# Optimization experiments

Measured on AMD Instinct MI355X. Metric: run time of the kernel, lower is better.

Reference implementation:

```python
import jax, jax.numpy as jnp
import numpy as np

B, C, H, W = 4, 288, 64, 64
P = 2
HEADS = 36
MLP_RATIO = 4.0
D = C * P * P              # hidden_size = 1152
HF = int(D * MLP_RATIO)    # 4608
LN_EPS = 1e-6
ATTN_EPS = 1e-8


def _layernorm(x):
    # LayerNorm over [C,H,W] per sample, no affine
    mu = jnp.mean(x, axis=(1, 2, 3), keepdims=True)
    var = jnp.mean((x - mu) ** 2, axis=(1, 2, 3), keepdims=True)
    return (x - mu) * jax.lax.rsqrt(var + LN_EPS)


def _seg(x):
    # b c (n1 p) (n2 p) -> b (n1 n2) (c p p)
    b, c, h, w = x.shape
    n1, n2 = h // P, w // P
    x = x.reshape(b, c, n1, P, n2, P).transpose(0, 2, 4, 1, 3, 5)
    return x.reshape(b, n1 * n2, c * P * P)


def _comb(t, h, w):
    # b (n1 n2) (c p p) -> b c (n1 p) (n2 p)
    b, n, dd = t.shape
    n1, n2 = h // P, w // P
    c = dd // (P * P)
    x = t.reshape(b, n1, n2, c, P, P).transpose(0, 3, 1, 4, 2, 5)
    return x.reshape(b, c, h, w)


def _lite_la(t, qkv_w, proj_w, proj_b):
    # ReLU-kernel linear attention with ones-padding normalization trick
    b, s, dm = t.shape
    d = dm // HEADS
    qkv = t @ qkv_w.T                       # [b,s,3*dm]
    q, k, v = jnp.split(qkv, 3, axis=-1)
    q = jax.nn.relu(q).reshape(b, s, HEADS, d)
    k = jax.nn.relu(k).reshape(b, s, HEADS, d)
    v = v.reshape(b, s, HEADS, d)
    v = jnp.concatenate([v, jnp.ones((b, s, HEADS, 1), v.dtype)], axis=-1)  # PAD_VAL=1
    vk = jnp.einsum('bshe,bshd->bhed', v, k)       # [b,h,d+1,d]
    out = jnp.einsum('bhed,bshd->bshe', vk, q)     # [b,s,h,d+1]
    out = out[..., :-1] / (out[..., -1:] + ATTN_EPS)
    return out.reshape(b, s, dm) @ proj_w.T + proj_b


def _glumb(t, inv_w, inv_b, dw_w, dw_b, pw_w):
    # GLU MBConv: 1x1 expand + SiLU -> 3x3 depthwise -> GLU gate -> 1x1 project
    b, n, c = t.shape
    hp = wp = int(n ** 0.5)
    x = t.reshape(b, hp, wp, c).transpose(0, 3, 1, 2)  # NCHW
    x = jnp.einsum('bchw,oc->bohw', x, inv_w[:, :, 0, 0]) + inv_b[None, :, None, None]
    x = jax.nn.silu(x)
    x = jax.lax.conv_general_dilated(x, dw_w, (1, 1), 'SAME',
                                     feature_group_count=dw_w.shape[0],
                                     dimension_numbers=('NCHW', 'OIHW', 'NCHW'))
    x = x + dw_b[None, :, None, None]
    x, gate = jnp.split(x, 2, axis=1)
    x = x * jax.nn.silu(gate)
    x = jnp.einsum('bchw,oc->bohw', x, pw_w[:, :, 0, 0])
    return x.reshape(b, c, n).transpose(0, 2, 1)


def setup_inputs() -> dict:
    key = jax.random.key(0)
    ks = jax.random.split(key, 10)
    s = 0.02
    return {
        'x': jax.random.normal(ks[0], (B, C, H, W), jnp.float32),
        'cond': jax.random.normal(ks[1], (B, 6 * C, H, W), jnp.float32),
        'global_token': jax.random.normal(ks[2], (B, D), jnp.float32),
        'time_token': jax.random.normal(ks[3], (B, D), jnp.float32),
        'ss_w': jax.random.normal(ks[4], (6 * C, 6 * C, 1, 1), jnp.float32) * s,
        'ss_b': jnp.zeros((6 * C,), jnp.float32),
        'qkv_w': jax.random.normal(ks[5], (3 * D, D), jnp.float32) * s,
        'proj_w': jax.random.normal(ks[6], (D, D), jnp.float32) * s,
        'proj_b': jnp.zeros((D,), jnp.float32),
        'inv_w': jax.random.normal(ks[7], (2 * HF, D, 1, 1), jnp.float32) * s,
        'inv_b': jnp.zeros((2 * HF,), jnp.float32),
        'dw_w': jax.random.normal(ks[8], (2 * HF, 1, 3, 3), jnp.float32) * s,
        'dw_b': jnp.zeros((2 * HF,), jnp.float32),
        'pw_w': jax.random.normal(ks[9], (D, HF, 1, 1), jnp.float32) * s,
    }


def reference(x, cond, global_token, time_token, ss_w, ss_b, qkv_w, proj_w, proj_b,
              inv_w, inv_b, dw_w, dw_b, pw_w):
    # scale_shift_table: SiLU + 1x1 conv on cond, chunk into 6 per-channel maps
    ss = jnp.einsum('bchw,oc->bohw', jax.nn.silu(cond), ss_w[:, :, 0, 0]) + ss_b[None, :, None, None]
    sh_msa, sc_msa, g_msa, sh_mlp, sc_mlp, g_mlp = jnp.split(ss, 6, axis=1)
    # attention branch
    tok = _seg(_layernorm(x) * (1.0 + sc_msa) + sh_msa)
    tok = jnp.concatenate([global_token[:, None], time_token[:, None], tok], axis=1)
    a = _lite_la(tok, qkv_w, proj_w, proj_b)
    x = x + _comb(a[:, 2:], H, W) * g_msa
    # MLP branch
    m = _glumb(_seg(_layernorm(x) * (1.0 + sc_mlp) + sh_mlp), inv_w, inv_b, dw_w, dw_b, pw_w)
    x = x + _comb(m, H, W) * g_mlp
    return x
```

## Files before the change

### kernel.cpp

```cpp
#include <hip/hip_runtime.h>
#include <hip/hip_bf16.h>
#include <cstdint>


typedef __bf16 bf16;
typedef bf16 bf16x8 __attribute__((ext_vector_type(8)));
typedef bf16 bf16x4 __attribute__((ext_vector_type(4)));
typedef float f32x4 __attribute__((ext_vector_type(4)));

typedef const __attribute__((address_space(1))) void gas_void;
typedef __attribute__((address_space(3))) void las_void;

__device__ __forceinline__ void gload16(const bf16* g, bf16* l) {
    __builtin_amdgcn_global_load_lds((gas_void*)g, (las_void*)l, 16, 0, 0);
}

#define BB 4
#define CC 288
#define HW 4096
#define C6 1728
#define DD 1152
#define SEQ 1026
#define RTOT 4104
#define NTOK 1024
#define HF 4608
#define HF2 9216
#define NPB 1179648

static constexpr size_t OFF_SUMS = 0;
static constexpr size_t OFF_SS   = 256;
static constexpr size_t SS_BYTES = (size_t)C6 * 16384 * 2;
static constexpr size_t OFF_R2   = OFF_SS + SS_BYTES;
static constexpr size_t OFF_PART1= OFF_R2;
static constexpr size_t OFF_A1   = OFF_R2;
static constexpr size_t OFF_T    = OFF_R2;
static constexpr size_t OFF_QKV  = OFF_T   + (size_t)RTOT*DD*2;
static constexpr size_t OFF_PART2= OFF_QKV;
static constexpr size_t OFF_VK   = OFF_QKV + (size_t)3456*RTOT*2;
static constexpr size_t OFF_ATT  = OFF_VK  + (size_t)144*1056*4;
static constexpr size_t OFF_APROJ= OFF_ATT + (size_t)RTOT*DD*2;
static constexpr size_t OFF_T2   = OFF_R2;
static constexpr size_t OFF_Y    = OFF_T2  + (size_t)4096*DD*2;
static constexpr size_t OFF_G    = OFF_Y   + (size_t)4096*HF2*2;
static constexpr size_t OFF_M    = OFF_G   + (size_t)4096*HF*2;
static constexpr size_t OFF_W    = OFF_R2  + 132120576;
static constexpr size_t OFF_WSS  = OFF_W;
static constexpr size_t OFF_WQKV = OFF_WSS  + (size_t)C6*C6*2;
static constexpr size_t OFF_WPROJ= OFF_WQKV + (size_t)3456*DD*2;
static constexpr size_t OFF_WINV = OFF_WPROJ+ (size_t)DD*DD*2;
static constexpr size_t OFF_WPW  = OFF_WINV + (size_t)HF2*DD*2;

__global__ __launch_bounds__(256) void cvt_bf16(const float* __restrict__ s,
                                                bf16* __restrict__ d, int n4) {
    int i = blockIdx.x * 256 + threadIdx.x;
    if (i < n4) {
        float4 v = ((const float4*)s)[i];
        bf16x4 o = {(bf16)v.x, (bf16)v.y, (bf16)v.z, (bf16)v.w};
        ((bf16x4*)d)[i] = o;
    }
}

__device__ __forceinline__ void block_reduce2_store(float s1, float s2, float* dst) {
    #pragma unroll
    for (int o = 32; o > 0; o >>= 1) { s1 += __shfl_down(s1, o); s2 += __shfl_down(s2, o); }
    __shared__ float r1[4], r2[4];
    int wave = threadIdx.x >> 6, lane = threadIdx.x & 63;
    if (lane == 0) { r1[wave] = s1; r2[wave] = s2; }
    __syncthreads();
    if (threadIdx.x == 0) {
        dst[0] = r1[0] + r1[1] + r1[2] + r1[3];
        dst[1] = r2[0] + r2[1] + r2[2] + r2[3];
    }
}

__global__ __launch_bounds__(256) void ln_stats(const float* __restrict__ x, float* __restrict__ part) {
    const float* base = x + (size_t)blockIdx.x * 4096;
    float s1 = 0.f, s2 = 0.f;
    #pragma unroll
    for (int it = 0; it < 4; it++) {
        float4 v = ((const float4*)base)[it * 256 + threadIdx.x];
        s1 += v.x + v.y + v.z + v.w;
        s2 += v.x * v.x + v.y * v.y + v.z * v.z + v.w * v.w;
    }
    block_reduce2_store(s1, s2, part + (size_t)blockIdx.x * 2);
}

__global__ __launch_bounds__(256) void reduce_part(const float* __restrict__ part, float* __restrict__ sums,
                                                   int nper, int out_off) {
    int b = blockIdx.x;
    float s1 = 0.f, s2 = 0.f;
    for (int i = threadIdx.x; i < nper; i += 256) {
        s1 += part[(size_t)(b * nper + i) * 2];
        s2 += part[(size_t)(b * nper + i) * 2 + 1];
    }
    block_reduce2_store(s1, s2, sums + out_off + b * 2);
}

__global__ __launch_bounds__(256) void prep_cond(const float* __restrict__ cond, bf16* __restrict__ A1) {
    __shared__ float tile[64][65];
    int b = blockIdx.z, k0 = blockIdx.y * 64, h0 = blockIdx.x * 64;
    int col = threadIdx.x & 63, r4 = threadIdx.x >> 6;
    const float* src = cond + ((size_t)b * C6 + k0) * HW + h0;
    #pragma unroll
    for (int p = 0; p < 16; p++) {
        int kk = r4 + p * 4;
        float v = src[(size_t)kk * HW + col];
        tile[col][kk] = v / (1.f + __expf(-v));
    }
    __syncthreads();
    bf16* dst = A1 + ((size_t)(b * HW + h0)) * C6 + k0;
    #pragma unroll
    for (int p = 0; p < 16; p++) {
        int rr = r4 + p * 4;
        dst[(size_t)rr * C6 + col] = (bf16)tile[rr][col];
    }
}

template <int EP, int BIAS>
__global__ __launch_bounds__(512, 2) void gemm256(const bf16* __restrict__ A, const bf16* __restrict__ B,
                                                  const float* __restrict__ bias, bf16* __restrict__ C,
                                                  int M, int N, int K, int reluLimit) {
    __shared__ __align__(16) bf16 As[2][256 * 64];
    __shared__ __align__(16) bf16 Bs[2][256 * 64];
    const int tid = threadIdx.x, wave = tid >> 6, lane = tid & 63;

    const int nx = gridDim.x, ny = gridDim.y, G = 8;
    int idx = blockIdx.y * nx + blockIdx.x;
    int total = nx * ny;
    int q = total >> 3, rm = total & 7;
    int xcd = idx & 7, slot = idx >> 3;
    int vid = (xcd < rm ? xcd * (q + 1) : rm * (q + 1) + (xcd - rm) * q) + slot;
    int band = vid / (G * nx);
    int r = vid - band * (G * nx);
    int gm = min(G, ny - band * G);
    const int m0 = (band * G + r % gm) * 256;
    const int n0 = (r / gm) * 256;

    const int srow_l = (wave << 3) + (lane >> 3);
    const int sk_el  = (((lane & 7) ^ (lane >> 3)) << 3);
    const bf16* pA[4]; const bf16* pB[4];
    #pragma unroll
    for (int g = 0; g < 4; ++g) {
        pA[g] = A + (size_t)min(m0 + g * 64 + srow_l, M - 1) * K + sk_el;
        pB[g] = B + (size_t)min(n0 + g * 64 + srow_l, N - 1) * K + sk_el;
    }
    auto STAGE_A = [&](int buf, int half) {
        #pragma unroll
        for (int rr = 0; rr < 2; ++rr) {
            gload16(pA[half * 2 + rr], &As[buf][half * 8192 + rr * 4096 + (wave << 9)]);
            pA[half * 2 + rr] += 64;
        }
    };
    auto STAGE_B = [&](int buf, int half) {
        #pragma unroll
        for (int rr = 0; rr < 2; ++rr) {
            gload16(pB[half * 2 + rr], &Bs[buf][half * 8192 + rr * 4096 + (wave << 9)]);
            pB[half * 2 + rr] += 64;
        }
    };

    const int wm_w = (wave >> 2) * 128, wn_w = (wave & 3) * 64;
    const int l15 = lane & 15;
    const int fswz = (l15 & 7) << 4;
    const int rk16 = (lane >> 4) << 4;

    bf16x8 af[8], bv[8];
    f32x4 acc[8][4];
    #pragma unroll
    for (int i = 0; i < 8; i++)
        #pragma unroll
        for (int j = 0; j < 4; j++) acc[i][j] = (f32x4){0.f, 0.f, 0.f, 0.f};

    auto LDA = [&](const bf16* base, int qm) {
        #pragma unroll
        for (int il = 0; il < 4; ++il)
            #pragma unroll
            for (int ks = 0; ks < 2; ++ks) {
                int row = wm_w + (qm * 4 + il) * 16 + l15;
                int kb  = (ks * 64 + rk16) ^ fswz;
                af[il * 2 + ks] = *(const bf16x8*)(base + row * 64 + (kb >> 1));
            }
    };
    auto LDB = [&](const bf16* base) {
        #pragma unroll
        for (int j = 0; j < 4; ++j)
            #pragma unroll
            for (int ks = 0; ks < 2; ++ks) {
                int row = wn_w + j * 16 + l15;
                int kb  = (ks * 64 + rk16) ^ fswz;
                bv[j * 2 + ks] = *(const bf16x8*)(base + row * 64 + (kb >> 1));
            }
    };
    auto MF = [&](int qm, int jh) {
        __builtin_amdgcn_s_setprio(1);
        #pragma unroll
        for (int il = 0; il < 4; ++il)
            #pragma unroll
            for (int jl = 0; jl < 2; ++jl)
                #pragma unroll
                for (int ks = 0; ks < 2; ++ks)
                    acc[qm * 4 + il][jh * 2 + jl] = __builtin_amdgcn_mfma_f32_16x16x32_bf16(
                        af[il * 2 + ks], bv[(jh * 2 + jl) * 2 + ks], acc[qm * 4 + il][jh * 2 + jl], 0, 0, 0);
        __builtin_amdgcn_s_setprio(0);
    };

    auto TILE = [&](int t, bool stage_next, bool last_vm) {
        const int cur = t & 1;
        const bf16* Ab = &As[cur][0];
        const bf16* Bb = &Bs[cur][0];
        LDA(Ab, 0);
        LDB(Bb);
        asm volatile("s_waitcnt lgkmcnt(0)" ::: "memory");
        __builtin_amdgcn_sched_barrier(0);
        __builtin_amdgcn_s_barrier();
        MF(0, 0);
        asm volatile("" ::: "memory");
        __builtin_amdgcn_s_barrier();
        asm volatile("" ::: "memory");
        if (stage_next) STAGE_B(cur, 0);
        asm volatile("" ::: "memory");
        __builtin_amdgcn_s_barrier();
        MF(0, 1);
        asm volatile("" ::: "memory");
        __builtin_amdgcn_s_barrier();
        asm volatile("" ::: "memory");
        LDA(Ab, 1);
        if (stage_next) STAGE_B(cur, 1);
        asm volatile("s_waitcnt lgkmcnt(0)" ::: "memory");
        __builtin_amdgcn_sched_barrier(0);
        __builtin_amdgcn_s_barrier();
        MF(1, 0);
        asm volatile("" ::: "memory");
        __builtin_amdgcn_s_barrier();
        asm volatile("" ::: "memory");
        if (stage_next) {
            STAGE_A(cur, 0); STAGE_A(cur, 1);
            asm volatile("s_waitcnt vmcnt(8)" ::: "memory");
            __builtin_amdgcn_sched_barrier(0);
        } else if (last_vm) {
            asm volatile("s_waitcnt vmcnt(0)" ::: "memory");
            __builtin_amdgcn_sched_barrier(0);
        }
        __builtin_amdgcn_s_barrier();
        MF(1, 1);
        asm volatile("" ::: "memory");
        __builtin_amdgcn_s_barrier();
        asm volatile("" ::: "memory");
    };

    const int nt = K >> 6;
    #pragma unroll
    for (int tt = 0; tt < 2; ++tt) {
        STAGE_B(tt, 0); STAGE_B(tt, 1);
        STAGE_A(tt, 0); STAGE_A(tt, 1);
    }
    asm volatile("s_waitcnt vmcnt(8)" ::: "memory");
    __builtin_amdgcn_sched_barrier(0);
    __builtin_amdgcn_s_barrier();
    asm volatile("" ::: "memory");
    for (int t = 0; t < nt - 2; ++t) TILE(t, true, false);
    TILE(nt - 2, false, true);
    TILE(nt - 1, false, false);

    const int mq = (lane >> 4) * 4, nl = lane & 15;
    #pragma unroll
    for (int i = 0; i < 8; i++) {
        #pragma unroll
        for (int j = 0; j < 4; j++) {
            int n = n0 + wn_w + j * 16 + nl;
            if (n < N) {
                #pragma unroll
                for (int r2 = 0; r2 < 4; r2++) {
                    int m = m0 + wm_w + i * 16 + mq + r2;
                    if (m < M) {
                        float v = acc[i][j][r2];
                        if (BIAS == 1) v += bias[m];
                        else if (BIAS == 2) v += bias[n];
                        if (EP == 1) { if (m < reluLimit) v = fmaxf(v, 0.f); }
                        else if (EP == 2) { v = v / (1.f + __expf(-v)); }
                        C[(size_t)m * N + n] = (bf16)v;
                    }
                }
            }
        }
    }
}

template <int EP, int BIAS>
__global__ __launch_bounds__(256) void gemm_bt(const bf16* __restrict__ A, const bf16* __restrict__ B,
                                               const float* __restrict__ bias, bf16* __restrict__ C,
                                               int M, int N, int K, int reluLimit) {
    __shared__ __align__(16) bf16 As[3][128 * 32];
    __shared__ __align__(16) bf16 Bs[3][128 * 32];
    const int tid = threadIdx.x, wave = tid >> 6, lane = tid & 63;

    const int nx = gridDim.x, ny = gridDim.y, G = 8;
    int idx = blockIdx.y * nx + blockIdx.x;
    int total = nx * ny;
    int q = total >> 3, rm = total & 7;
    int xcd = idx & 7, slot = idx >> 3;
    int vid = (xcd < rm ? xcd * (q + 1) : rm * (q + 1) + (xcd - rm) * q) + slot;
    int band = vid / (G * nx);
    int r = vid - band * (G * nx);
    int gm = min(G, ny - band * G);
    const int m0 = (band * G + r % gm) * 128;
    const int n0 = (r / gm) * 128;

    const int c0 = wave * 128 + lane;
    const int c1 = c0 + 64;
    const int sw = ((c0 >> 2) & 3) ^ ((c0 >> 4) & 3);
    const int ka = (((c0 & 3) ^ sw)) * 8;
    int ra0 = min(m0 + (c0 >> 2), M - 1), ra1 = min(m0 + (c1 >> 2), M - 1);
    int rb0 = min(n0 + (c0 >> 2), N - 1), rb1 = min(n0 + (c1 >> 2), N - 1);
    const bf16* gA0 = A + (size_t)ra0 * K + ka;
    const bf16* gA1 = A + (size_t)ra1 * K + ka;
    const bf16* gB0 = B + (size_t)rb0 * K + ka;
    const bf16* gB1 = B + (size_t)rb1 * K + ka;

    const int wm = (wave >> 1) * 64, wn = (wave & 1) * 64;
    const int l15 = lane & 15;
    const int sr = (l15 & 3) ^ ((l15 >> 2) & 3);
    const int fc = ((lane >> 4) ^ sr) * 8;
    const int fao = (wm + l15) * 32 + fc;
    const int fbo = (wn + l15) * 32 + fc;
    const int lwo = wave * 1024;

    f32x4 acc[4][4];
    #pragma unroll
    for (int i = 0; i < 4; i++)
        #pragma unroll
        for (int j = 0; j < 4; j++) acc[i][j] = (f32x4){0.f, 0.f, 0.f, 0.f};

    auto STAGE = [&](int buf) {
        gload16(gA0, &As[buf][lwo]);
        gload16(gA1, &As[buf][lwo + 512]);
        gload16(gB0, &Bs[buf][lwo]);
        gload16(gB1, &Bs[buf][lwo + 512]);
        gA0 += 32; gA1 += 32; gB0 += 32; gB1 += 32;
    };
    auto COMP = [&](int buf) {
        const bf16* fa = &As[buf][fao];
        const bf16* fb = &Bs[buf][fbo];
        bf16x8 af[4], bvv[4];
        #pragma unroll
        for (int i = 0; i < 4; i++) af[i] = *(const bf16x8*)(fa + i * 16 * 32);
        #pragma unroll
        for (int j = 0; j < 4; j++) bvv[j] = *(const bf16x8*)(fb + j * 16 * 32);
        #pragma unroll
        for (int i = 0; i < 4; i++)
            #pragma unroll
            for (int j = 0; j < 4; j++)
                acc[i][j] = __builtin_amdgcn_mfma_f32_16x16x32_bf16(af[i], bvv[j], acc[i][j], 0, 0, 0);
    };
    auto STEP = [&](int cbuf, int sbuf) {
        STAGE(sbuf);
        asm volatile("s_waitcnt vmcnt(8)" ::: "memory");
        __builtin_amdgcn_s_barrier();
        asm volatile("" ::: "memory");
        COMP(cbuf);
        asm volatile("" ::: "memory");
        __builtin_amdgcn_s_barrier();
    };

    const int nt = K >> 5;
    STAGE(0);
    STAGE(1);
    for (int it = 0; it < nt / 3 - 1; ++it) {
        STEP(0, 2);
        STEP(1, 0);
        STEP(2, 1);
    }
    STEP(0, 2);
    asm volatile("s_waitcnt vmcnt(4)" ::: "memory");
    __builtin_amdgcn_s_barrier();
    asm volatile("" ::: "memory");
    COMP(1);
    asm volatile("" ::: "memory");
    asm volatile("s_waitcnt vmcnt(0)" ::: "memory");
    __builtin_amdgcn_s_barrier();
    asm volatile("" ::: "memory");
    COMP(2);

    const int mq = (lane >> 4) * 4, nl = lane & 15;
    #pragma unroll
    for (int i = 0; i < 4; i++) {
        #pragma unroll
        for (int j = 0; j < 4; j++) {
            int n = n0 + wn + j * 16 + nl;
            if (n < N) {
                #pragma unroll
                for (int r2 = 0; r2 < 4; r2++) {
                    int m = m0 + wm + i * 16 + mq + r2;
                    if (m < M) {
                        float v = acc[i][j][r2];
                        if (BIAS == 1) v += bias[m];
                        else if (BIAS == 2) v += bias[n];
                        if (EP == 1) { if (m < reluLimit) v = fmaxf(v, 0.f); }
                        else if (EP == 2) { v = v / (1.f + __expf(-v)); }
                        C[(size_t)m * N + n] = (bf16)v;
                    }
                }
            }
        }
    }
}

__global__ __launch_bounds__(256) void build_tok_t(const float* __restrict__ xs, const bf16* __restrict__ ss,
                                                   const float* __restrict__ sums, int soff, int shb, int scb,
                                                   bf16* __restrict__ dst, int tokoff, int seqstride) {
    __shared__ bf16 tl[32][132];
    int cch = blockIdx.x, n1 = blockIdx.y, b = blockIdx.z;
    int c0 = cch * 32;
    int tid = threadIdx.x, cl = tid >> 3, wseg = tid & 7;

    float mu = sums[soff + b * 2] * (1.f / (float)NPB);
    float var = sums[soff + b * 2 + 1] * (1.f / (float)NPB) - mu * mu;
    float rsig = rsqrtf(var + 1e-6f);

    int c = c0 + cl;
    #pragma unroll
    for (int hh = 0; hh < 2; hh++) {
        int hw = (2 * n1 + hh) * 64 + wseg * 8;
        const float* xp = xs + ((size_t)b * CC + c) * HW + hw;
        float4 x0 = ((const float4*)xp)[0];
        float4 x1 = ((const float4*)xp)[1];
        bf16x8 scv = *(const bf16x8*)(ss + (size_t)(scb + c) * 16384 + b * HW + hw);
        bf16x8 shv = *(const bf16x8*)(ss + (size_t)(shb + c) * 16384 + b * HW + hw);
        float xv[8] = {x0.x, x0.y, x0.z, x0.w, x1.x, x1.y, x1.z, x1.w};
        #pragma unroll
        for (int k = 0; k < 8; k++) {
            int w = wseg * 8 + k;
            float v = (xv[k] - mu) * rsig * (1.f + (float)scv[k]) + (float)shv[k];
            tl[w >> 1][cl * 4 + hh * 2 + (w & 1)] = (bf16)v;
        }
    }
    __syncthreads();
    int token = tid >> 3, seg = (tid & 7) * 16;
    bf16* drow = dst + ((size_t)(b * seqstride + tokoff + n1 * 32 + token)) * DD + c0 * 4 + seg;
    *(bf16x8*)drow = *(const bf16x8*)&tl[token][seg];
    *(bf16x8*)(drow + 8) = *(const bf16x8*)&tl[token][seg + 8];
}

__global__ __launch_bounds__(256) void copy_gt(const float* __restrict__ gtok, const float* __restrict__ ttok,
                                               bf16* __restrict__ T) {
    int which = blockIdx.x, b = blockIdx.y;
    const float* src = (which == 0 ? gtok : ttok) + b * DD;
    bf16* dst = T + (size_t)(b * SEQ + which) * DD;
    for (int d = threadIdx.x; d < DD; d += 256) dst[d] = (bf16)src[d];
}

__global__ __launch_bounds__(256) void attn_vk(const bf16* __restrict__ qkv, float* __restrict__ vk) {
    int bh = blockIdx.x >> 2, sb = blockIdx.x & 3;
    int b = bh / 36, h = bh % 36;
    int s_begin = sb * 288;
    int s_end = min(s_begin + 288, SEQ);
    const bf16* kbase = qkv + (size_t)(DD + h * 32) * RTOT + b * SEQ;
    const bf16* vbase = qkv + (size_t)(2 * DD + h * 32) * RTOT + b * SEQ;
    __shared__ __align__(16) bf16 kk[32][80];
    __shared__ __align__(16) bf16 vv[32][80];
    int tid = threadIdx.x;
    int e = tid >> 3, dg = (tid & 7) * 4;
    int lrow = tid >> 3, lcol = (tid & 7) * 8;
    float a0 = 0.f, a1 = 0.f, a2 = 0.f, a3 = 0.f, aD = 0.f;
    for (int s0 = s_begin; s0 < s_end; s0 += 64) {
        __syncthreads();
        #pragma unroll
        for (int j = 0; j < 8; j++) {
            int s = s0 + lcol + j;
            bool ok = s < s_end;
            kk[lrow][lcol + j] = ok ? kbase[(size_t)lrow * RTOT + s] : (bf16)0.f;
            vv[lrow][lcol + j] = ok ? vbase[(size_t)lrow * RTOT + s] : (bf16)0.f;
        }
        __syncthreads();
        #pragma unroll
        for (int j0 = 0; j0 < 64; j0 += 8) {
            bf16x8 vvv = *(const bf16x8*)&vv[e][j0];
            bf16x8 k0 = *(const bf16x8*)&kk[dg + 0][j0];
            bf16x8 k1 = *(const bf16x8*)&kk[dg + 1][j0];
            bf16x8 k2 = *(const bf16x8*)&kk[dg + 2][j0];
            bf16x8 k3 = *(const bf16x8*)&kk[dg + 3][j0];
            #pragma unroll
            for (int j = 0; j < 8; j++) {
                float vf = (float)vvv[j];
                a0 += vf * (float)k0[j];
                a1 += vf * (float)k1[j];
                a2 += vf * (float)k2[j];
                a3 += vf * (float)k3[j];
            }
            if (tid < 32) {
                bf16x8 kd = *(const bf16x8*)&kk[tid][j0];
                #pragma unroll
                for (int j = 0; j < 8; j++) aD += (float)kd[j];
            }
        }
    }
    float* dst = vk + (size_t)bh * 1056;
    atomicAdd(&dst[e * 32 + dg + 0], a0);
    atomicAdd(&dst[e * 32 + dg + 1], a1);
    atomicAdd(&dst[e * 32 + dg + 2], a2);
    atomicAdd(&dst[e * 32 + dg + 3], a3);
    if (tid < 32) atomicAdd(&dst[1024 + tid], aD);
}

__global__ __launch_bounds__(256) void attn_out(const bf16* __restrict__ qkv, const float* __restrict__ vk,
                                                bf16* __restrict__ att) {
    int bh = blockIdx.y, b = bh / 36, h = bh % 36;
    int s0 = blockIdx.x * 64;
    __shared__ float vks[1056];
    __shared__ __align__(16) bf16 qs[32][80];
    int tid = threadIdx.x;
    for (int i = tid; i < 1056; i += 256) vks[i] = vk[(size_t)bh * 1056 + i];
    const bf16* qbase = qkv + (size_t)(h * 32) * RTOT + b * SEQ;
    int lrow = tid >> 3, lcol = (tid & 7) * 8;
    #pragma unroll
    for (int j = 0; j < 8; j++) {
        int s = s0 + lcol + j;
        qs[lrow][lcol + j] = (s < SEQ) ? qbase[(size_t)lrow * RTOT + s] : (bf16)0.f;
    }
    __syncthreads();
    int sl = tid >> 2, eg = (tid & 3) * 8;
    int s = s0 + sl;
    float num[8] = {0.f, 0.f, 0.f, 0.f, 0.f, 0.f, 0.f, 0.f};
    float den = 0.f;
    #pragma unroll
    for (int d = 0; d < 32; d++) {
        float qv = (float)qs[d][sl];
        den += vks[1024 + d] * qv;
        #pragma unroll
        for (int t = 0; t < 8; t++) num[t] += vks[(eg + t) * 32 + d] * qv;
    }
    if (s < SEQ) {
        float inv = 1.f / (den + 1e-8f);
        bf16* dst = att + ((size_t)(b * SEQ + s)) * DD + h * 32 + eg;
        #pragma unroll
        for (int t = 0; t < 8; t++) dst[t] = (bf16)(num[t] * inv);
    }
}

__global__ __launch_bounds__(256) void add_attn(const float* __restrict__ x, const bf16* __restrict__ aproj,
                                                const bf16* __restrict__ ss, float* __restrict__ xo,
                                                float* __restrict__ part) {
    int b = blockIdx.x / 4608;
    size_t idx = (size_t)blockIdx.x * 256 + threadIdx.x;
    size_t local = idx - (size_t)b * NPB;
    int c = (int)(local >> 12), hw = (int)(local & 4095);
    int hh = hw >> 6, w = hw & 63;
    int n = (hh >> 1) * 32 + (w >> 1);
    int dd = c * 4 + (hh & 1) * 2 + (w & 1);
    float a = (float)aproj[(size_t)dd * RTOT + b * SEQ + 2 + n];
    float g = (float)ss[(size_t)(576 + c) * 16384 + b * HW + hw];
    float v = x[idx] + a * g;
    xo[idx] = v;
    block_reduce2_store(v, v * v, part + (size_t)blockIdx.x * 2);
}

__global__ __launch_bounds__(256) void dwglu(const bf16* __restrict__ y, const float* __restrict__ dw_w,
                                             const float* __restrict__ dw_b, bf16* __restrict__ g) {
    __shared__ __align__(16) bf16 xs[6400];
    __shared__ __align__(16) bf16 gs[6400];
    int b = blockIdx.z, tile = blockIdx.y, c0 = blockIdx.x * 64;
    int ty = (tile >> 2) * 8, tx = (tile & 3) * 8;
    int tid = threadIdx.x, cc = tid & 63, pg = tid >> 6;
    int pos8 = tid >> 3, cseg = (tid & 7) * 8;
    bf16x8 z = {(bf16)0.f, (bf16)0.f, (bf16)0.f, (bf16)0.f,
                (bf16)0.f, (bf16)0.f, (bf16)0.f, (bf16)0.f};
    #pragma unroll
    for (int p0 = 0; p0 < 128; p0 += 32) {
        int p = p0 + pos8;
        if (p < 100) {
            int py = ty + p / 10 - 1, px = tx + p % 10 - 1;
            bool in = (py >= 0 && py < 32 && px >= 0 && px < 32);
            bf16x8 xv = z, gv = z;
            if (in) {
                size_t base = ((size_t)(b * NTOK + py * 32 + px)) * HF2 + c0 + cseg;
                xv = *(const bf16x8*)&y[base];
                gv = *(const bf16x8*)&y[base + HF];
            }
            *(bf16x8*)&xs[p * 64 + cseg] = xv;
            *(bf16x8*)&gs[p * 64 + cseg] = gv;
        }
    }
    float wx[9], wg[9];
    #pragma unroll
    for (int t = 0; t < 9; t++) {
        wx[t] = dw_w[(size_t)(c0 + cc) * 9 + t];
        wg[t] = dw_w[(size_t)(HF + c0 + cc) * 9 + t];
    }
    float bx = dw_b[c0 + cc], bg = dw_b[HF + c0 + cc];
    __syncthreads();
    for (int p = pg * 16; p < pg * 16 + 16; p++) {
        int py = p >> 3, px = p & 7;
        float ax = bx, ag = bg;
        #pragma unroll
        for (int dy = 0; dy < 3; dy++)
            #pragma unroll
            for (int dx = 0; dx < 3; dx++) {
                int q = (py + dy) * 10 + (px + dx);
                ax += (float)xs[q * 64 + cc] * wx[dy * 3 + dx];
                ag += (float)gs[q * 64 + cc] * wg[dy * 3 + dx];
            }
        float out = ax * (ag / (1.f + __expf(-ag)));
        g[((size_t)(b * NTOK + (ty + py) * 32 + tx + px)) * HF + c0 + cc] = (bf16)out;
    }
}

__global__ __launch_bounds__(256) void add_mlp(const bf16* __restrict__ mm, const bf16* __restrict__ ss,
                                               float* __restrict__ xo) {
    int b = blockIdx.x / 4608;
    size_t idx = (size_t)blockIdx.x * 256 + threadIdx.x;
    size_t local = idx - (size_t)b * NPB;
    int c = (int)(local >> 12), hw = (int)(local & 4095);
    int hh = hw >> 6, w = hw & 63;
    int n = (hh >> 1) * 32 + (w >> 1);
    int dd = c * 4 + (hh & 1) * 2 + (w & 1);
    float mv = (float)mm[(size_t)dd * 4096 + b * NTOK + n];
    float g = (float)ss[(size_t)(1440 + c) * 16384 + b * HW + hw];
    xo[idx] = xo[idx] + mv * g;
}

extern "C" void kernel_launch(void* const* d_in, const int* in_sizes, int n_in,
                              void* d_out, int out_size, void* d_ws, size_t ws_size,
                              hipStream_t stream) {
    (void)in_sizes; (void)n_in; (void)out_size; (void)ws_size;
    const float* x      = (const float*)d_in[0];
    const float* cond   = (const float*)d_in[1];
    const float* gtok   = (const float*)d_in[2];
    const float* ttok   = (const float*)d_in[3];
    const float* ss_w   = (const float*)d_in[4];
    const float* ss_b   = (const float*)d_in[5];
    const float* qkv_w  = (const float*)d_in[6];
    const float* proj_w = (const float*)d_in[7];
    const float* proj_b = (const float*)d_in[8];
    const float* inv_w  = (const float*)d_in[9];
    const float* inv_b  = (const float*)d_in[10];
    const float* dw_w   = (const float*)d_in[11];
    const float* dw_b   = (const float*)d_in[12];
    const float* pw_w   = (const float*)d_in[13];
    float* out = (float*)d_out;
    char* ws = (char*)d_ws;

    float* sums  = (float*)(ws + OFF_SUMS);
    float* PART1 = (float*)(ws + OFF_PART1);
    float* PART2 = (float*)(ws + OFF_PART2);
    bf16* SS    = (bf16*)(ws + OFF_SS);
    bf16* A1    = (bf16*)(ws + OFF_A1);
    bf16* T     = (bf16*)(ws + OFF_T);
    bf16* QKV   = (bf16*)(ws + OFF_QKV);
    float* VK   = (float*)(ws + OFF_VK);
    bf16* ATT   = (bf16*)(ws + OFF_ATT);
    bf16* APROJ = (bf16*)(ws + OFF_APROJ);
    bf16* T2    = (bf16*)(ws + OFF_T2);
    bf16* Y     = (bf16*)(ws + OFF_Y);
    bf16* G     = (bf16*)(ws + OFF_G);
    bf16* MM    = (bf16*)(ws + OFF_M);
    bf16* WSS   = (bf16*)(ws + OFF_WSS);
    bf16* WQKV  = (bf16*)(ws + OFF_WQKV);
    bf16* WPROJ = (bf16*)(ws + OFF_WPROJ);
    bf16* WINV  = (bf16*)(ws + OFF_WINV);
    bf16* WPW   = (bf16*)(ws + OFF_WPW);

    cvt_bf16<<<2916, 256, 0, stream>>>(ss_w, WSS, C6 * C6 / 4);
    cvt_bf16<<<3888, 256, 0, stream>>>(qkv_w, WQKV, 3456 * DD / 4);
    cvt_bf16<<<1296, 256, 0, stream>>>(proj_w, WPROJ, DD * DD / 4);
    cvt_bf16<<<10368, 256, 0, stream>>>(inv_w, WINV, HF2 * DD / 4);
    cvt_bf16<<<5184, 256, 0, stream>>>(pw_w, WPW, DD * HF / 4);

    ln_stats<<<1152, 256, 0, stream>>>(x, PART1);
    reduce_part<<<4, 256, 0, stream>>>(PART1, sums, 288, 0);
    prep_cond<<<dim3(64, 27, 4), 256, 0, stream>>>(cond, A1);
    gemm256<0, 1><<<dim3(64, 7), 512, 0, stream>>>(WSS, A1, ss_b, SS, C6, 16384, C6, 0);
    build_tok_t<<<dim3(9, 32, 4), 256, 0, stream>>>(x, SS, sums, 0, 0, 288, T, 2, SEQ);
    copy_gt<<<dim3(2, 4), 256, 0, stream>>>(gtok, ttok, T);
    gemm256<1, 0><<<dim3(17, 14), 512, 0, stream>>>(WQKV, T, nullptr, QKV, 3456, RTOT, DD, 2304);
    hipMemsetAsync(ws + OFF_VK, 0, (size_t)144 * 1056 * 4, stream);
    attn_vk<<<576, 256, 0, stream>>>(QKV, VK);
    attn_out<<<dim3(17, 144), 256, 0, stream>>>(QKV, VK, ATT);
    gemm_bt<0, 1><<<dim3(33, 9), 256, 0, stream>>>(WPROJ, ATT, proj_b, APROJ, DD, RTOT, DD, 0);
    add_attn<<<18432, 256, 0, stream>>>(x, APROJ, SS, out, PART2);
    reduce_part<<<4, 256, 0, stream>>>(PART2, sums, 4608, 8);
    build_tok_t<<<dim3(9, 32, 4), 256, 0, stream>>>(out, SS, sums, 8, 864, 1152, T2, 0, 1024);
    gemm256<2, 2><<<dim3(36, 16), 512, 0, stream>>>(T2, WINV, inv_b, Y, 4096, HF2, DD, 0);
    dwglu<<<dim3(72, 16, 4), 256, 0, stream>>>(Y, dw_w, dw_b, G);
    gemm_bt<0, 0><<<dim3(32, 9), 256, 0, stream>>>(WPW, G, nullptr, MM, DD, 4096, HF, 0);
    add_mlp<<<18432, 256, 0, stream>>>(MM, SS, out);
}
```

Before: 1.065 ms.

## Simplify GEMM main loop to two barriers per K tile with reordered prefetch

```diff
diff --git a/kernel.cpp b/kernel.cpp
--- a/kernel.cpp
+++ b/kernel.cpp
@@ -191,76 +191,49 @@
                 bv[j * 2 + ks] = *(const bf16x8*)(base + row * 64 + (kb >> 1));
             }
     };
-    auto MF = [&](int qm, int jh) {
+    auto MFQ = [&](int qm) {
         __builtin_amdgcn_s_setprio(1);
         #pragma unroll
         for (int il = 0; il < 4; ++il)
             #pragma unroll
-            for (int jl = 0; jl < 2; ++jl)
+            for (int j = 0; j < 4; ++j)
                 #pragma unroll
                 for (int ks = 0; ks < 2; ++ks)
-                    acc[qm * 4 + il][jh * 2 + jl] = __builtin_amdgcn_mfma_f32_16x16x32_bf16(
-                        af[il * 2 + ks], bv[(jh * 2 + jl) * 2 + ks], acc[qm * 4 + il][jh * 2 + jl], 0, 0, 0);
+                    acc[qm * 4 + il][j] = __builtin_amdgcn_mfma_f32_16x16x32_bf16(
+                        af[il * 2 + ks], bv[j * 2 + ks], acc[qm * 4 + il][j], 0, 0, 0);
         __builtin_amdgcn_s_setprio(0);
     };
 
-    auto TILE = [&](int t, bool stage_next, bool last_vm) {
-        const int cur = t & 1;
+    const int nt = K >> 6;
+    STAGE_B(0, 0); STAGE_B(0, 1); STAGE_A(0, 0); STAGE_A(0, 1);
+    STAGE_B(1, 0); STAGE_B(1, 1); STAGE_A(1, 0); STAGE_A(1, 1);
+    asm volatile("s_waitcnt vmcnt(8)" ::: "memory");
+    __builtin_amdgcn_s_barrier();
+    asm volatile("" ::: "memory");
+
+    for (int t = 0; t < nt; ++t) {
+        const int cur = t & 1, oth = cur ^ 1;
         const bf16* Ab = &As[cur][0];
         const bf16* Bb = &Bs[cur][0];
         LDA(Ab, 0);
         LDB(Bb);
-        asm volatile("s_waitcnt lgkmcnt(0)" ::: "memory");
-        __builtin_amdgcn_sched_barrier(0);
-        __builtin_amdgcn_s_barrier();
-        MF(0, 0);
-        asm volatile("" ::: "memory");
-        __builtin_amdgcn_s_barrier();
-        asm volatile("" ::: "memory");
-        if (stage_next) STAGE_B(cur, 0);
-        asm volatile("" ::: "memory");
-        __builtin_amdgcn_s_barrier();
-        MF(0, 1);
+        if (t >= 1 && t + 1 < nt) { STAGE_A(oth, 0); STAGE_A(oth, 1); }
+        MFQ(0);
         asm volatile("" ::: "memory");
         __builtin_amdgcn_s_barrier();
         asm volatile("" ::: "memory");
         LDA(Ab, 1);
-        if (stage_next) STAGE_B(cur, 1);
-        asm volatile("s_waitcnt lgkmcnt(0)" ::: "memory");
-        __builtin_amdgcn_sched_barrier(0);
-        __builtin_amdgcn_s_barrier();
-        MF(1, 0);
+        if (t + 2 < nt) {
+            STAGE_B(cur, 0); STAGE_B(cur, 1);
+            asm volatile("s_waitcnt vmcnt(4)" ::: "memory");
+        } else if (t + 2 == nt) {
+            asm volatile("s_waitcnt vmcnt(0)" ::: "memory");
+        }
+        MFQ(1);
         asm volatile("" ::: "memory");
         __builtin_amdgcn_s_barrier();
         asm volatile("" ::: "memory");
-        if (stage_next) {
-            STAGE_A(cur, 0); STAGE_A(cur, 1);
-            asm volatile("s_waitcnt vmcnt(8)" ::: "memory");
-            __builtin_amdgcn_sched_barrier(0);
-        } else if (last_vm) {
-            asm volatile("s_waitcnt vmcnt(0)" ::: "memory");
-            __builtin_amdgcn_sched_barrier(0);
-        }
-        __builtin_amdgcn_s_barrier();
-        MF(1, 1);
-        asm volatile("" ::: "memory");
-        __builtin_amdgcn_s_barrier();
-        asm volatile("" ::: "memory");
-    };
-
-    const int nt = K >> 6;
-    #pragma unroll
-    for (int tt = 0; tt < 2; ++tt) {
-        STAGE_B(tt, 0); STAGE_B(tt, 1);
-        STAGE_A(tt, 0); STAGE_A(tt, 1);
-    }
-    asm volatile("s_waitcnt vmcnt(8)" ::: "memory");
-    __builtin_amdgcn_sched_barrier(0);
-    __builtin_amdgcn_s_barrier();
-    asm volatile("" ::: "memory");
-    for (int t = 0; t < nt - 2; ++t) TILE(t, true, false);
-    TILE(nt - 2, false, true);
-    TILE(nt - 1, false, false);
+    }
 
     const int mq = (lane >> 4) * 4, nl = lane & 15;
     #pragma unroll
```

Measured after the change: 1.015 ms. 4.7% less time.
